# Kernel optimization log

Hardware: AMD Instinct MI355X
Metric: run time of the kernel (lower is better)

## Reference

```python
import jax, jax.numpy as jnp
import numpy as np

N_NODES = 50000


def gcn_conv(x, W, b, src, dst, n_nodes):
    # PyG GCNConv: y = D^-1/2 (A + I) D^-1/2 (x @ W) + b, with D counting self-loops
    h = x @ W                                             # [N, out]
    deg = jnp.ones((n_nodes,), h.dtype).at[dst].add(1.0)  # in-degree + self-loop
    dinv = jax.lax.rsqrt(deg)
    norm = dinv[src] * dinv[dst]                          # [E]
    msg = h[src] * norm[:, None]                          # [E, out]
    out = jnp.zeros_like(h).at[dst].add(msg)              # scatter-add over edges
    out = out + h * (dinv * dinv)[:, None]                # self-loop contribution
    return out + b


def setup_inputs() -> dict:
    key = jax.random.key(0)
    k = jax.random.split(key, 7)
    d_in, d_hid, d_out = 128, 128, 64
    x = jax.random.normal(k[0], (N_NODES, d_in), jnp.float32)
    edge_index = jax.random.randint(k[1], (2, 800000), 0, N_NODES, jnp.int64)
    s1 = 1.0 / np.sqrt(d_in)
    s2 = 1.0 / np.sqrt(d_hid)
    W1 = jax.random.uniform(k[2], (d_in, d_hid), jnp.float32, -s1, s1)
    b1 = jnp.zeros((d_hid,), jnp.float32)
    W2 = jax.random.uniform(k[3], (d_hid, d_out), jnp.float32, -s2, s2)
    b2 = jnp.zeros((d_out,), jnp.float32)
    return {"x": x, "edge_index": edge_index, "W1": W1, "b1": b1, "W2": W2, "b2": b2}


def reference(x, edge_index, W1, b1, W2, b2):
    src, dst = edge_index[0], edge_index[1]
    h = jax.nn.relu(gcn_conv(x, W1, b1, src, dst, N_NODES))
    h = gcn_conv(h, W2, b2, src, dst, N_NODES)
    return jax.nn.log_softmax(h, axis=1)
```

## Files before the change

kernel.cpp:

```cpp
#include <hip/hip_runtime.h>
#include <hip/hip_bf16.h>
#include <math.h>


typedef unsigned int uint32;
typedef unsigned short ushort16;
typedef __attribute__((ext_vector_type(8))) short bf16x8;
typedef __attribute__((ext_vector_type(4))) float f32x4;

__device__ inline unsigned short f2bf_rne(float f) {
    uint32 x = __float_as_uint(f);
    uint32 r = (x + 0x7fffu + ((x >> 16) & 1u)) >> 16;
    return (unsigned short)r;
}
__device__ inline uint32 pack_bf16x2(float a, float b) {
    return (uint32)f2bf_rne(a) | ((uint32)f2bf_rne(b) << 16);
}
__device__ inline float2 unpack_bf16x2(uint32 u) {
    float2 r;
    r.x = __uint_as_float(u << 16);
    r.y = __uint_as_float(u & 0xffff0000u);
    return r;
}

#define NHB 128

__global__ __launch_bounds__(256) void hist_conv_k(const int* __restrict__ dst, int E,
                                                   int NW, int chunk,
                                                   uint32* __restrict__ counts_pb,
                                                   ushort16* __restrict__ rankx,
                                                   const float* __restrict__ W1,
                                                   const float* __restrict__ W2,
                                                   unsigned short* __restrict__ W1t,
                                                   unsigned short* __restrict__ W2t) {
    const int tid = threadIdx.x;
    if ((int)blockIdx.x >= NHB) {
        int idx = ((int)blockIdx.x - NHB) * 256 + tid;
        if (idx < 128 * 128) {
            int ns = idx >> 7, k = idx & 127;
            int t = ns >> 4, m = ns & 15;
            int col = 32 * (t >> 1) + 2 * m + (t & 1);
            W1t[idx] = f2bf_rne(W1[k * 128 + col]);
        } else {
            int i2 = idx - 128 * 128;
            if (i2 < 64 * 128) {
                int ns = i2 >> 7, k = i2 & 127;
                int t = ns >> 4, m = ns & 15;
                int col = 32 * (t >> 1) + 2 * m + (t & 1);
                W2t[i2] = f2bf_rne(W2[k * 64 + col]);
            }
        }
        return;
    }
    extern __shared__ uint32 sh[];
    const int b = blockIdx.x;
    for (int i = tid; i < NW; i += 256) sh[i] = 0;
    __syncthreads();
    const int e0 = b * chunk;
    const int e1 = min(E, e0 + chunk);
    int e = e0 + tid;
    for (; e + 768 < e1; e += 1024) {
        int d0 = dst[e];
        int d1 = dst[e + 256];
        int d2 = dst[e + 512];
        int d3 = dst[e + 768];
        uint32 o0 = atomicAdd(&sh[d0 >> 1], (d0 & 1) ? 0x10000u : 1u);
        uint32 o1 = atomicAdd(&sh[d1 >> 1], (d1 & 1) ? 0x10000u : 1u);
        uint32 o2 = atomicAdd(&sh[d2 >> 1], (d2 & 1) ? 0x10000u : 1u);
        uint32 o3 = atomicAdd(&sh[d3 >> 1], (d3 & 1) ? 0x10000u : 1u);
        rankx[e]       = (ushort16)((d0 & 1) ? (o0 >> 16) : (o0 & 0xffffu));
        rankx[e + 256] = (ushort16)((d1 & 1) ? (o1 >> 16) : (o1 & 0xffffu));
        rankx[e + 512] = (ushort16)((d2 & 1) ? (o2 >> 16) : (o2 & 0xffffu));
        rankx[e + 768] = (ushort16)((d3 & 1) ? (o3 >> 16) : (o3 & 0xffffu));
    }
    for (; e < e1; e += 256) {
        int d = dst[e];
        uint32 o = atomicAdd(&sh[d >> 1], (d & 1) ? 0x10000u : 1u);
        rankx[e] = (ushort16)((d & 1) ? (o >> 16) : (o & 0xffffu));
    }
    __syncthreads();
    uint32* dstp = counts_pb + (size_t)b * NW;
    for (int i = tid; i < NW; i += 256) dstp[i] = sh[i];
}

__global__ __launch_bounds__(256) void scan2_k(const uint32* __restrict__ counts_pb,
                                               int N, int NW,
                                               ushort16* __restrict__ basecum,
                                               int* __restrict__ exscan,
                                               int* __restrict__ blocksum,
                                               float* __restrict__ dinv) {
    __shared__ int sd[256];
    const int tid = threadIdx.x;
    const int n   = blockIdx.x * 256 + tid;
    const int nc  = n < N ? n : N - 1;
    const int w   = nc >> 1;
    const bool hi = (nc & 1) != 0;
    int cum = 0;
    for (int bb = 0; bb < NHB; bb += 16) {
        uint32 wv[16];
#pragma unroll
        for (int j = 0; j < 16; ++j)
            wv[j] = counts_pb[(size_t)(bb + j) * NW + w];
#pragma unroll
        for (int j = 0; j < 16; ++j) {
            int c = hi ? (int)(wv[j] >> 16) : (int)(wv[j] & 0xffffu);
            if (n < N) basecum[(size_t)(bb + j) * N + n] = (ushort16)cum;
            cum += c;
        }
    }
    int v = (n < N) ? cum : 0;
    if (n < N) dinv[n] = rsqrtf((float)(v + 1));
    sd[tid] = v;
    __syncthreads();
    for (int off = 1; off < 256; off <<= 1) {
        int t = (tid >= off) ? sd[tid - off] : 0;
        __syncthreads();
        sd[tid] += t;
        __syncthreads();
    }
    if (n < N) exscan[n] = sd[tid] - v;
    if (tid == 255) blocksum[blockIdx.x] = sd[255];
}

__global__ __launch_bounds__(256) void fill_gemm1_k(const int* __restrict__ src,
                                                    const int* __restrict__ dst, int E,
                                                    int chunk, int N,
                                                    const ushort16* __restrict__ rankx,
                                                    const ushort16* __restrict__ basecum,
                                                    const int* __restrict__ blocksum,
                                                    int NB,
                                                    const int* __restrict__ exscan,
                                                    int* __restrict__ offsets,
                                                    ushort16* __restrict__ csr_src,
                                                    const float* __restrict__ X,
                                                    const unsigned short* __restrict__ Wt,
                                                    const float* __restrict__ dinv,
                                                    uint32* __restrict__ Yu, int Nrows) {
    __shared__ int sd[256];
    __shared__ int ebs[256];
    __shared__ int total;
    if ((int)blockIdx.x < 256) {
        const int f   = blockIdx.x;
        const int tid = threadIdx.x;
        int v = (tid < NB) ? blocksum[tid] : 0;
        sd[tid] = v;
        __syncthreads();
        for (int off = 1; off < 256; off <<= 1) {
            int t = (tid >= off) ? sd[tid - off] : 0;
            __syncthreads();
            sd[tid] += t;
            __syncthreads();
        }
        ebs[tid] = sd[tid] - v;
        if (tid == 255) total = sd[255];
        __syncthreads();
        int g = f * 256 + tid;
        if (g < N) offsets[g] = ebs[g >> 8] + exscan[g];
        else if (g == N) offsets[N] = total;
        const int b  = f >> 1;
        const ushort16* bc = basecum + (size_t)b * N;
        const int q2 = chunk >> 1;
        const int e0 = b * chunk + (f & 1) * q2;
        const int e1 = min(E, e0 + q2);
        int e = e0 + tid;
        for (; e + 768 < e1; e += 1024) {
#pragma unroll
            for (int j = 0; j < 4; ++j) {
                int ej = e + j * 256;
                int d = dst[ej];
                int pos = ebs[d >> 8] + exscan[d] + (int)bc[d] + (int)rankx[ej];
                csr_src[pos] = (ushort16)src[ej];
            }
        }
        for (; e < e1; e += 256) {
            int d = dst[e];
            int pos = ebs[d >> 8] + exscan[d] + (int)bc[d] + (int)rankx[e];
            csr_src[pos] = (ushort16)src[e];
        }
        return;
    }
    constexpr int NCOL = 128;
    constexpr int NT = NCOL / 16;
    const int tid  = threadIdx.x;
    const int wave = tid >> 6;
    const int lane = tid & 63;
    const int m16  = lane & 15;
    const int q    = lane >> 4;
    const int r0   = ((int)blockIdx.x - 256) * 64 + wave * 16;

    int arow = r0 + m16;
    if (arow >= Nrows) arow = Nrows - 1;

    bf16x8 afrag[4];
#pragma unroll
    for (int kb = 0; kb < 4; ++kb) {
        const float* p = &X[(size_t)arow * 128 + kb * 32 + q * 8];
        float4 u0 = *(const float4*)p;
        float4 u1 = *(const float4*)(p + 4);
        bf16x8 a;
        a[0] = (short)f2bf_rne(u0.x); a[1] = (short)f2bf_rne(u0.y);
        a[2] = (short)f2bf_rne(u0.z); a[3] = (short)f2bf_rne(u0.w);
        a[4] = (short)f2bf_rne(u1.x); a[5] = (short)f2bf_rne(u1.y);
        a[6] = (short)f2bf_rne(u1.z); a[7] = (short)f2bf_rne(u1.w);
        afrag[kb] = a;
    }

    f32x4 acc[NT];
#pragma unroll
    for (int t = 0; t < NT; ++t) acc[t] = (f32x4){0.f, 0.f, 0.f, 0.f};
#pragma unroll
    for (int t = 0; t < NT; ++t) {
        const unsigned short* Bp = &Wt[(size_t)(t * 16 + m16) * 128 + q * 8];
#pragma unroll
        for (int kb = 0; kb < 4; ++kb) {
            bf16x8 bfrag = *(const bf16x8*)&Bp[kb * 32];
            acc[t] = __builtin_amdgcn_mfma_f32_16x16x32_bf16(afrag[kb], bfrag, acc[t], 0, 0, 0);
        }
    }
#pragma unroll
    for (int i = 0; i < 4; ++i) {
        int row = r0 + q * 4 + i;
        if (row < Nrows) {
            float dn = dinv[row];
#pragma unroll
            for (int u = 0; u < NT / 2; ++u)
                Yu[(size_t)row * (NCOL / 2) + u * 16 + m16] =
                    pack_bf16x2(acc[2 * u][i] * dn, acc[2 * u + 1][i] * dn);
        }
    }
}

__global__ __launch_bounds__(256, 8) void agg1_gemm2_k(const unsigned short* __restrict__ hs,
                                                       const int* __restrict__ offsets,
                                                       const ushort16* __restrict__ csr_src,
                                                       const float* __restrict__ dinv,
                                                       const float* __restrict__ b1,
                                                       const unsigned short* __restrict__ W2t,
                                                       uint32* __restrict__ Yu, int N) {
    __shared__ uint32 srow[16 * 68];
    const int tid  = threadIdx.x;
    const int w    = tid >> 6;
    const int lane = tid & 63;
    const int base = (int)blockIdx.x * 16;
    const uint32* T = (const uint32*)hs;
    const float2 bb = ((const float2*)b1)[lane];
#pragma unroll
    for (int which = 0; which < 4; ++which) {
        const int node = base + 4 * w + which;
        uint32 packed = 0;
        if (node < N) {
            const int start = offsets[node];
            const int end   = offsets[node + 1];
            const float dn  = dinv[node];
            float2 self = unpack_bf16x2(T[(size_t)node * 64 + lane]);
            float ax0 = self.x, ay0 = self.y;
            float ax1 = 0.f, ay1 = 0.f, ax2 = 0.f, ay2 = 0.f, ax3 = 0.f, ay3 = 0.f;
            int p = start;
            for (; p + 7 < end; p += 8) {
                int s0 = csr_src[p];
                int s1 = csr_src[p + 1];
                int s2 = csr_src[p + 2];
                int s3 = csr_src[p + 3];
                int s4 = csr_src[p + 4];
                int s5 = csr_src[p + 5];
                int s6 = csr_src[p + 6];
                int s7 = csr_src[p + 7];
                uint32 u0 = T[(size_t)s0 * 64 + lane];
                uint32 u1 = T[(size_t)s1 * 64 + lane];
                uint32 u2 = T[(size_t)s2 * 64 + lane];
                uint32 u3 = T[(size_t)s3 * 64 + lane];
                uint32 u4 = T[(size_t)s4 * 64 + lane];
                uint32 u5 = T[(size_t)s5 * 64 + lane];
                uint32 u6 = T[(size_t)s6 * 64 + lane];
                uint32 u7 = T[(size_t)s7 * 64 + lane];
                float2 f0 = unpack_bf16x2(u0);
                float2 f1 = unpack_bf16x2(u1);
                float2 f2 = unpack_bf16x2(u2);
                float2 f3 = unpack_bf16x2(u3);
                float2 f4 = unpack_bf16x2(u4);
                float2 f5 = unpack_bf16x2(u5);
                float2 f6 = unpack_bf16x2(u6);
                float2 f7 = unpack_bf16x2(u7);
                ax0 += f0.x + f4.x; ay0 += f0.y + f4.y;
                ax1 += f1.x + f5.x; ay1 += f1.y + f5.y;
                ax2 += f2.x + f6.x; ay2 += f2.y + f6.y;
                ax3 += f3.x + f7.x; ay3 += f3.y + f7.y;
            }
            for (; p + 3 < end; p += 4) {
                int s0 = csr_src[p];
                int s1 = csr_src[p + 1];
                int s2 = csr_src[p + 2];
                int s3 = csr_src[p + 3];
                float2 f0 = unpack_bf16x2(T[(size_t)s0 * 64 + lane]);
                float2 f1 = unpack_bf16x2(T[(size_t)s1 * 64 + lane]);
                float2 f2 = unpack_bf16x2(T[(size_t)s2 * 64 + lane]);
                float2 f3 = unpack_bf16x2(T[(size_t)s3 * 64 + lane]);
                ax0 += f0.x; ay0 += f0.y;
                ax1 += f1.x; ay1 += f1.y;
                ax2 += f2.x; ay2 += f2.y;
                ax3 += f3.x; ay3 += f3.y;
            }
            for (; p < end; ++p) {
                float2 f = unpack_bf16x2(T[(size_t)csr_src[p] * 64 + lane]);
                ax1 += f.x; ay1 += f.y;
            }
            float vx = ((ax0 + ax1) + (ax2 + ax3)) * dn + bb.x;
            float vy = ((ay0 + ay1) + (ay2 + ay3)) * dn + bb.y;
            vx = vx > 0.f ? vx : 0.f;
            vy = vy > 0.f ? vy : 0.f;
            packed = pack_bf16x2(vx, vy);
        }
        srow[(4 * w + which) * 68 + lane] = packed;
    }
    __syncthreads();
    if (w < 2) {
        const int pp  = w;
        const int m16 = lane & 15;
        const int q   = lane >> 4;
        bf16x8 afrag[4];
#pragma unroll
        for (int kb = 0; kb < 4; ++kb)
            afrag[kb] = *(const bf16x8*)&srow[m16 * 68 + kb * 16 + q * 4];
        f32x4 acc0 = (f32x4){0.f, 0.f, 0.f, 0.f};
        f32x4 acc1 = (f32x4){0.f, 0.f, 0.f, 0.f};
        const unsigned short* Bp0 = &W2t[(size_t)((2 * pp) * 16 + m16) * 128 + q * 8];
        const unsigned short* Bp1 = &W2t[(size_t)((2 * pp + 1) * 16 + m16) * 128 + q * 8];
#pragma unroll
        for (int kb = 0; kb < 4; ++kb) {
            bf16x8 b0  = *(const bf16x8*)&Bp0[kb * 32];
            bf16x8 b1f = *(const bf16x8*)&Bp1[kb * 32];
            acc0 = __builtin_amdgcn_mfma_f32_16x16x32_bf16(afrag[kb], b0, acc0, 0, 0, 0);
            acc1 = __builtin_amdgcn_mfma_f32_16x16x32_bf16(afrag[kb], b1f, acc1, 0, 0, 0);
        }
#pragma unroll
        for (int i = 0; i < 4; ++i) {
            int row = base + q * 4 + i;
            if (row < N) {
                float dn2 = dinv[row];
                Yu[(size_t)row * 32 + pp * 16 + m16] =
                    pack_bf16x2(acc0[i] * dn2, acc1[i] * dn2);
            }
        }
    }
}

__global__ __launch_bounds__(256) void agg2_k(const unsigned short* __restrict__ hs,
                                              const int* __restrict__ offsets,
                                              const ushort16* __restrict__ csr_src,
                                              const float* __restrict__ dinv,
                                              const float* __restrict__ b2,
                                              float* __restrict__ out, int N) {
    const int tid  = threadIdx.x;
    const int node = blockIdx.x * 8 + (tid >> 5);
    const int l    = tid & 31;
    if (node >= N) return;
    const uint32* T = (const uint32*)hs;
    const int start = offsets[node];
    const int end   = offsets[node + 1];
    const float dn  = dinv[node];
    float2 self = unpack_bf16x2(T[(size_t)node * 32 + l]);
    float ax0 = self.x, ay0 = self.y;
    float ax1 = 0.f, ay1 = 0.f, ax2 = 0.f, ay2 = 0.f, ax3 = 0.f, ay3 = 0.f;
    int p = start;
    for (; p + 7 < end; p += 8) {
        int s0 = csr_src[p];
        int s1 = csr_src[p + 1];
        int s2 = csr_src[p + 2];
        int s3 = csr_src[p + 3];
        int s4 = csr_src[p + 4];
        int s5 = csr_src[p + 5];
        int s6 = csr_src[p + 6];
        int s7 = csr_src[p + 7];
        uint32 u0 = T[(size_t)s0 * 32 + l];
        uint32 u1 = T[(size_t)s1 * 32 + l];
        uint32 u2 = T[(size_t)s2 * 32 + l];
        uint32 u3 = T[(size_t)s3 * 32 + l];
        uint32 u4 = T[(size_t)s4 * 32 + l];
        uint32 u5 = T[(size_t)s5 * 32 + l];
        uint32 u6 = T[(size_t)s6 * 32 + l];
        uint32 u7 = T[(size_t)s7 * 32 + l];
        float2 f0 = unpack_bf16x2(u0);
        float2 f1 = unpack_bf16x2(u1);
        float2 f2 = unpack_bf16x2(u2);
        float2 f3 = unpack_bf16x2(u3);
        float2 f4 = unpack_bf16x2(u4);
        float2 f5 = unpack_bf16x2(u5);
        float2 f6 = unpack_bf16x2(u6);
        float2 f7 = unpack_bf16x2(u7);
        ax0 += f0.x + f4.x; ay0 += f0.y + f4.y;
        ax1 += f1.x + f5.x; ay1 += f1.y + f5.y;
        ax2 += f2.x + f6.x; ay2 += f2.y + f6.y;
        ax3 += f3.x + f7.x; ay3 += f3.y + f7.y;
    }
    for (; p + 3 < end; p += 4) {
        int s0 = csr_src[p];
        int s1 = csr_src[p + 1];
        int s2 = csr_src[p + 2];
        int s3 = csr_src[p + 3];
        float2 f0 = unpack_bf16x2(T[(size_t)s0 * 32 + l]);
        float2 f1 = unpack_bf16x2(T[(size_t)s1 * 32 + l]);
        float2 f2 = unpack_bf16x2(T[(size_t)s2 * 32 + l]);
        float2 f3 = unpack_bf16x2(T[(size_t)s3 * 32 + l]);
        ax0 += f0.x; ay0 += f0.y;
        ax1 += f1.x; ay1 += f1.y;
        ax2 += f2.x; ay2 += f2.y;
        ax3 += f3.x; ay3 += f3.y;
    }
    for (; p < end; ++p) {
        float2 f = unpack_bf16x2(T[(size_t)csr_src[p] * 32 + l]);
        ax1 += f.x; ay1 += f.y;
    }
    float2 bb = ((const float2*)b2)[l];
    float vx = ((ax0 + ax1) + (ax2 + ax3)) * dn + bb.x;
    float vy = ((ay0 + ay1) + (ay2 + ay3)) * dn + bb.y;
    float m = fmaxf(vx, vy);
#pragma unroll
    for (int off = 16; off > 0; off >>= 1) m = fmaxf(m, __shfl_xor(m, off, 64));
    float ex = __expf(vx - m) + __expf(vy - m);
    float ssum = ex;
#pragma unroll
    for (int off = 16; off > 0; off >>= 1) ssum += __shfl_xor(ssum, off, 64);
    float lse = m + __logf(ssum);
    float2 o = {vx - lse, vy - lse};
    ((float2*)out)[(size_t)node * 32 + l] = o;
}

extern "C" void kernel_launch(void* const* d_in, const int* in_sizes, int n_in,
                              void* d_out, int out_size, void* d_ws, size_t ws_size,
                              hipStream_t stream) {
    const float* x  = (const float*)d_in[0];
    const int*   ei = (const int*)d_in[1];
    const float* W1 = (const float*)d_in[2];
    const float* b1 = (const float*)d_in[3];
    const float* W2 = (const float*)d_in[4];
    const float* b2 = (const float*)d_in[5];
    float* out = (float*)d_out;

    const int N = in_sizes[0] / 128;
    const int E = in_sizes[1] / 2;
    const int* src = ei;
    const int* dst = ei + E;
    const int NB = (N + 255) / 256;
    const int NW = (N + 1) / 2;
    const int chunk = (E + NHB - 1) / NHB;

    char* ws = (char*)d_ws;
    auto alloc = [&](size_t bytes) -> char* {
        char* p = ws;
        ws += (bytes + 255) & ~(size_t)255;
        return p;
    };
    unsigned short* h1  = (unsigned short*)alloc((size_t)N * 128 * 2);
    unsigned short* h2  = (unsigned short*)alloc((size_t)N * 64 * 2);
    uint32* counts_pb = (uint32*)alloc((size_t)NHB * NW * 4);
    ushort16* basecum = (ushort16*)alloc((size_t)NHB * N * 2);
    ushort16* rankx   = (ushort16*)alloc((size_t)E * 2);
    ushort16* csr_src = (ushort16*)alloc((size_t)E * 2);
    float* dinv     = (float*)alloc((size_t)N * 4);
    int*   exscan   = (int*)alloc((size_t)N * 4);
    int*   blocksum = (int*)alloc((size_t)NB * 4);
    int*   offsets  = (int*)alloc((size_t)(N + 1) * 4);
    unsigned short* W1t = (unsigned short*)alloc(128 * 128 * 2);
    unsigned short* W2t = (unsigned short*)alloc(64 * 128 * 2);

    const int GB = (N + 63) / 64;
    const int CB = (128 * 128 + 64 * 128 + 255) / 256;

    hist_conv_k<<<NHB + CB, 256, NW * 4, stream>>>(dst, E, NW, chunk, counts_pb, rankx,
                                                   W1, W2, W1t, W2t);
    scan2_k<<<NB, 256, 0, stream>>>(counts_pb, N, NW, basecum, exscan, blocksum, dinv);
    fill_gemm1_k<<<256 + GB, 256, 0, stream>>>(src, dst, E, chunk, N, rankx, basecum,
                                               blocksum, NB, exscan, offsets, csr_src,
                                               x, W1t, dinv, (uint32*)h1, N);
    agg1_gemm2_k<<<(N + 15) / 16, 256, 0, stream>>>(h1, offsets, csr_src, dinv, b1,
                                                    W2t, (uint32*)h2, N);
    agg2_k<<<(N + 7) / 8, 256, 0, stream>>>(h2, offsets, csr_src, dinv, b2, out, N);
}
```

Before: 191.6 us.

## Pad CSR rows to multiples of 8 with a zero dummy node and quarter histogram shared memory

```diff
diff --git a/kernel.cpp b/kernel.cpp
--- a/kernel.cpp
+++ b/kernel.cpp
@@ -34,8 +34,8 @@
                                                    unsigned short* __restrict__ W1t,
                                                    unsigned short* __restrict__ W2t) {
     const int tid = threadIdx.x;
-    if ((int)blockIdx.x >= NHB) {
-        int idx = ((int)blockIdx.x - NHB) * 256 + tid;
+    if ((int)blockIdx.x >= 4 * NHB) {
+        int idx = ((int)blockIdx.x - 4 * NHB) * 256 + tid;
         if (idx < 128 * 128) {
             int ns = idx >> 7, k = idx & 127;
             int t = ns >> 4, m = ns & 15;
@@ -53,10 +53,15 @@
         return;
     }
     extern __shared__ uint32 sh[];
-    const int b = blockIdx.x;
-    for (int i = tid; i < NW; i += 256) sh[i] = 0;
+    const int hb  = blockIdx.x >> 2;
+    const int qt  = blockIdx.x & 3;
+    const int NWq = (NW + 3) >> 2;
+    const int qlo = qt * NWq;
+    const int qhi = min(NW, qlo + NWq);
+    const int qn  = qhi - qlo;
+    for (int i = tid; i < qn; i += 256) sh[i] = 0;
     __syncthreads();
-    const int e0 = b * chunk;
+    const int e0 = hb * chunk;
     const int e1 = min(E, e0 + chunk);
     int e = e0 + tid;
     for (; e + 768 < e1; e += 1024) {
@@ -64,23 +69,35 @@
         int d1 = dst[e + 256];
         int d2 = dst[e + 512];
         int d3 = dst[e + 768];
-        uint32 o0 = atomicAdd(&sh[d0 >> 1], (d0 & 1) ? 0x10000u : 1u);
-        uint32 o1 = atomicAdd(&sh[d1 >> 1], (d1 & 1) ? 0x10000u : 1u);
-        uint32 o2 = atomicAdd(&sh[d2 >> 1], (d2 & 1) ? 0x10000u : 1u);
-        uint32 o3 = atomicAdd(&sh[d3 >> 1], (d3 & 1) ? 0x10000u : 1u);
-        rankx[e]       = (ushort16)((d0 & 1) ? (o0 >> 16) : (o0 & 0xffffu));
-        rankx[e + 256] = (ushort16)((d1 & 1) ? (o1 >> 16) : (o1 & 0xffffu));
-        rankx[e + 512] = (ushort16)((d2 & 1) ? (o2 >> 16) : (o2 & 0xffffu));
-        rankx[e + 768] = (ushort16)((d3 & 1) ? (o3 >> 16) : (o3 & 0xffffu));
+        int w0 = d0 >> 1, w1 = d1 >> 1, w2 = d2 >> 1, w3 = d3 >> 1;
+        if (w0 >= qlo && w0 < qhi) {
+            uint32 o = atomicAdd(&sh[w0 - qlo], (d0 & 1) ? 0x10000u : 1u);
+            rankx[e] = (ushort16)((d0 & 1) ? (o >> 16) : (o & 0xffffu));
+        }
+        if (w1 >= qlo && w1 < qhi) {
+            uint32 o = atomicAdd(&sh[w1 - qlo], (d1 & 1) ? 0x10000u : 1u);
+            rankx[e + 256] = (ushort16)((d1 & 1) ? (o >> 16) : (o & 0xffffu));
+        }
+        if (w2 >= qlo && w2 < qhi) {
+            uint32 o = atomicAdd(&sh[w2 - qlo], (d2 & 1) ? 0x10000u : 1u);
+            rankx[e + 512] = (ushort16)((d2 & 1) ? (o >> 16) : (o & 0xffffu));
+        }
+        if (w3 >= qlo && w3 < qhi) {
+            uint32 o = atomicAdd(&sh[w3 - qlo], (d3 & 1) ? 0x10000u : 1u);
+            rankx[e + 768] = (ushort16)((d3 & 1) ? (o >> 16) : (o & 0xffffu));
+        }
     }
     for (; e < e1; e += 256) {
         int d = dst[e];
-        uint32 o = atomicAdd(&sh[d >> 1], (d & 1) ? 0x10000u : 1u);
-        rankx[e] = (ushort16)((d & 1) ? (o >> 16) : (o & 0xffffu));
+        int w = d >> 1;
+        if (w >= qlo && w < qhi) {
+            uint32 o = atomicAdd(&sh[w - qlo], (d & 1) ? 0x10000u : 1u);
+            rankx[e] = (ushort16)((d & 1) ? (o >> 16) : (o & 0xffffu));
+        }
     }
     __syncthreads();
-    uint32* dstp = counts_pb + (size_t)b * NW;
-    for (int i = tid; i < NW; i += 256) dstp[i] = sh[i];
+    uint32* dstp = counts_pb + (size_t)hb * NW + qlo;
+    for (int i = tid; i < qn; i += 256) dstp[i] = sh[i];
 }
 
 __global__ __launch_bounds__(256) void scan2_k(const uint32* __restrict__ counts_pb,
@@ -88,7 +105,8 @@
                                                ushort16* __restrict__ basecum,
                                                int* __restrict__ exscan,
                                                int* __restrict__ blocksum,
-                                               float* __restrict__ dinv) {
+                                               float* __restrict__ dinv,
+                                               ushort16* __restrict__ degs) {
     __shared__ int sd[256];
     const int tid = threadIdx.x;
     const int n   = blockIdx.x * 256 + tid;
@@ -109,8 +127,12 @@
         }
     }
     int v = (n < N) ? cum : 0;
-    if (n < N) dinv[n] = rsqrtf((float)(v + 1));
-    sd[tid] = v;
+    if (n < N) {
+        dinv[n] = rsqrtf((float)(v + 1));
+        degs[n] = (ushort16)v;
+    }
+    int vp = (v + 7) & ~7;
+    sd[tid] = vp;
     __syncthreads();
     for (int off = 1; off < 256; off <<= 1) {
         int t = (tid >= off) ? sd[tid - off] : 0;
@@ -118,7 +140,7 @@
         sd[tid] += t;
         __syncthreads();
     }
-    if (n < N) exscan[n] = sd[tid] - v;
+    if (n < N) exscan[n] = sd[tid] - vp;
     if (tid == 255) blocksum[blockIdx.x] = sd[255];
 }
 
@@ -130,6 +152,7 @@
                                                     const int* __restrict__ blocksum,
                                                     int NB,
                                                     const int* __restrict__ exscan,
+                                                    const ushort16* __restrict__ degs,
                                                     int* __restrict__ offsets,
                                                     ushort16* __restrict__ csr_src,
                                                     const float* __restrict__ X,
@@ -155,8 +178,15 @@
         if (tid == 255) total = sd[255];
         __syncthreads();
         int g = f * 256 + tid;
-        if (g < N) offsets[g] = ebs[g >> 8] + exscan[g];
-        else if (g == N) offsets[N] = total;
+        if (g < N) {
+            int off = ebs[g >> 8] + exscan[g];
+            offsets[g] = off;
+            int dg = degs[g];
+            int pl = (dg + 7) & ~7;
+            for (int k = dg; k < pl; ++k) csr_src[off + k] = (ushort16)N;
+        } else if (g == N) {
+            offsets[N] = total;
+        }
         const int b  = f >> 1;
         const ushort16* bc = basecum + (size_t)b * N;
         const int q2 = chunk >> 1;
@@ -187,6 +217,8 @@
     const int m16  = lane & 15;
     const int q    = lane >> 4;
     const int r0   = ((int)blockIdx.x - 256) * 64 + wave * 16;
+
+    if ((int)blockIdx.x == 256 && tid < 64) Yu[(size_t)Nrows * (NCOL / 2) + tid] = 0;
 
     int arow = r0 + m16;
     if (arow >= Nrows) arow = Nrows - 1;
@@ -244,6 +276,7 @@
     const int base = (int)blockIdx.x * 16;
     const uint32* T = (const uint32*)hs;
     const float2 bb = ((const float2*)b1)[lane];
+    if (blockIdx.x == 0 && w == 2 && lane < 32) Yu[(size_t)N * 32 + lane] = 0;
 #pragma unroll
     for (int which = 0; which < 4; ++which) {
         const int node = base + 4 * w + which;
@@ -256,15 +289,17 @@
             float ax0 = self.x, ay0 = self.y;
             float ax1 = 0.f, ay1 = 0.f, ax2 = 0.f, ay2 = 0.f, ax3 = 0.f, ay3 = 0.f;
             int p = start;
-            for (; p + 7 < end; p += 8) {
-                int s0 = csr_src[p];
-                int s1 = csr_src[p + 1];
-                int s2 = csr_src[p + 2];
-                int s3 = csr_src[p + 3];
-                int s4 = csr_src[p + 4];
-                int s5 = csr_src[p + 5];
-                int s6 = csr_src[p + 6];
-                int s7 = csr_src[p + 7];
+            for (; p + 15 < end; p += 16) {
+                uint4 ia = *(const uint4*)&csr_src[p];
+                uint4 ib = *(const uint4*)&csr_src[p + 8];
+                int s0 = ia.x & 0xffff, s1 = ia.x >> 16;
+                int s2 = ia.y & 0xffff, s3 = ia.y >> 16;
+                int s4 = ia.z & 0xffff, s5 = ia.z >> 16;
+                int s6 = ia.w & 0xffff, s7 = ia.w >> 16;
+                int s8 = ib.x & 0xffff, s9 = ib.x >> 16;
+                int sa = ib.y & 0xffff, sb = ib.y >> 16;
+                int sc = ib.z & 0xffff, sd = ib.z >> 16;
+                int se = ib.w & 0xffff, sf = ib.w >> 16;
                 uint32 u0 = T[(size_t)s0 * 64 + lane];
                 uint32 u1 = T[(size_t)s1 * 64 + lane];
                 uint32 u2 = T[(size_t)s2 * 64 + lane];
@@ -273,36 +308,53 @@
                 uint32 u5 = T[(size_t)s5 * 64 + lane];
                 uint32 u6 = T[(size_t)s6 * 64 + lane];
                 uint32 u7 = T[(size_t)s7 * 64 + lane];
-                float2 f0 = unpack_bf16x2(u0);
-                float2 f1 = unpack_bf16x2(u1);
-                float2 f2 = unpack_bf16x2(u2);
-                float2 f3 = unpack_bf16x2(u3);
-                float2 f4 = unpack_bf16x2(u4);
-                float2 f5 = unpack_bf16x2(u5);
-                float2 f6 = unpack_bf16x2(u6);
-                float2 f7 = unpack_bf16x2(u7);
+                uint32 u8 = T[(size_t)s8 * 64 + lane];
+                uint32 u9 = T[(size_t)s9 * 64 + lane];
+                uint32 ua = T[(size_t)sa * 64 + lane];
+                uint32 ub = T[(size_t)sb * 64 + lane];
+                uint32 uc = T[(size_t)sc * 64 + lane];
+                uint32 ud = T[(size_t)sd * 64 + lane];
+                uint32 ue = T[(size_t)se * 64 + lane];
+                uint32 uf = T[(size_t)sf * 64 + lane];
+                float2 f0 = unpack_bf16x2(u0), f1 = unpack_bf16x2(u1);
+                float2 f2 = unpack_bf16x2(u2), f3 = unpack_bf16x2(u3);
+                float2 f4 = unpack_bf16x2(u4), f5 = unpack_bf16x2(u5);
+                float2 f6 = unpack_bf16x2(u6), f7 = unpack_bf16x2(u7);
+                float2 f8 = unpack_bf16x2(u8), f9 = unpack_bf16x2(u9);
+                float2 fa = unpack_bf16x2(ua), fb = unpack_bf16x2(ub);
+                float2 fc = unpack_bf16x2(uc), fd = unpack_bf16x2(ud);
+                float2 fe = unpack_bf16x2(ue), ff = unpack_bf16x2(uf);
+                ax0 += (f0.x + f4.x) + (f8.x + fc.x);
+                ay0 += (f0.y + f4.y) + (f8.y + fc.y);
+                ax1 += (f1.x + f5.x) + (f9.x + fd.x);
+                ay1 += (f1.y + f5.y) + (f9.y + fd.y);
+                ax2 += (f2.x + f6.x) + (fa.x + fe.x);
+                ay2 += (f2.y + f6.y) + (fa.y + fe.y);
+                ax3 += (f3.x + f7.x) + (fb.x + ff.x);
+                ay3 += (f3.y + f7.y) + (fb.y + ff.y);
+            }
+            for (; p + 7 < end; p += 8) {
+                uint4 ia = *(const uint4*)&csr_src[p];
+                int s0 = ia.x & 0xffff, s1 = ia.x >> 16;
+                int s2 = ia.y & 0xffff, s3 = ia.y >> 16;
+                int s4 = ia.z & 0xffff, s5 = ia.z >> 16;
+                int s6 = ia.w & 0xffff, s7 = ia.w >> 16;
+                uint32 u0 = T[(size_t)s0 * 64 + lane];
+                uint32 u1 = T[(size_t)s1 * 64 + lane];
+                uint32 u2 = T[(size_t)s2 * 64 + lane];
+                uint32 u3 = T[(size_t)s3 * 64 + lane];
+                uint32 u4 = T[(size_t)s4 * 64 + lane];
+                uint32 u5 = T[(size_t)s5 * 64 + lane];
+                uint32 u6 = T[(size_t)s6 * 64 + lane];
+                uint32 u7 = T[(size_t)s7 * 64 + lane];
+                float2 f0 = unpack_bf16x2(u0), f1 = unpack_bf16x2(u1);
+                float2 f2 = unpack_bf16x2(u2), f3 = unpack_bf16x2(u3);
+                float2 f4 = unpack_bf16x2(u4), f5 = unpack_bf16x2(u5);
+                float2 f6 = unpack_bf16x2(u6), f7 = unpack_bf16x2(u7);
                 ax0 += f0.x + f4.x; ay0 += f0.y + f4.y;
                 ax1 += f1.x + f5.x; ay1 += f1.y + f5.y;
                 ax2 += f2.x + f6.x; ay2 += f2.y + f6.y;
                 ax3 += f3.x + f7.x; ay3 += f3.y + f7.y;
-            }
-            for (; p + 3 < end; p += 4) {
-                int s0 = csr_src[p];
-                int s1 = csr_src[p + 1];
-                int s2 = csr_src[p + 2];
-                int s3 = csr_src[p + 3];
-                float2 f0 = unpack_bf16x2(T[(size_t)s0 * 64 + lane]);
-                float2 f1 = unpack_bf16x2(T[(size_t)s1 * 64 + lane]);
-                float2 f2 = unpack_bf16x2(T[(size_t)s2 * 64 + lane]);
-                float2 f3 = unpack_bf16x2(T[(size_t)s3 * 64 + lane]);
-                ax0 += f0.x; ay0 += f0.y;
-                ax1 += f1.x; ay1 += f1.y;
-                ax2 += f2.x; ay2 += f2.y;
-                ax3 += f3.x; ay3 += f3.y;
-            }
-            for (; p < end; ++p) {
-                float2 f = unpack_bf16x2(T[(size_t)csr_src[p] * 64 + lane]);
-                ax1 += f.x; ay1 += f.y;
             }
             float vx = ((ax0 + ax1) + (ax2 + ax3)) * dn + bb.x;
             float vy = ((ay0 + ay1) + (ay2 + ay3)) * dn + bb.y;
@@ -344,12 +396,12 @@
     }
 }
 
-__global__ __launch_bounds__(256) void agg2_k(const unsigned short* __restrict__ hs,
-                                              const int* __restrict__ offsets,
-                                              const ushort16* __restrict__ csr_src,
-                                              const float* __restrict__ dinv,
-                                              const float* __restrict__ b2,
-                                              float* __restrict__ out, int N) {
+__global__ __launch_bounds__(256, 8) void agg2_k(const unsigned short* __restrict__ hs,
+                                                 const int* __restrict__ offsets,
+                                                 const ushort16* __restrict__ csr_src,
+                                                 const float* __restrict__ dinv,
+                                                 const float* __restrict__ b2,
+                                                 float* __restrict__ out, int N) {
     const int tid  = threadIdx.x;
     const int node = blockIdx.x * 8 + (tid >> 5);
     const int l    = tid & 31;
@@ -362,15 +414,17 @@
     float ax0 = self.x, ay0 = self.y;
     float ax1 = 0.f, ay1 = 0.f, ax2 = 0.f, ay2 = 0.f, ax3 = 0.f, ay3 = 0.f;
     int p = start;
-    for (; p + 7 < end; p += 8) {
-        int s0 = csr_src[p];
-        int s1 = csr_src[p + 1];
-        int s2 = csr_src[p + 2];
-        int s3 = csr_src[p + 3];
-        int s4 = csr_src[p + 4];
-        int s5 = csr_src[p + 5];
-        int s6 = csr_src[p + 6];
-        int s7 = csr_src[p + 7];
+    for (; p + 15 < end; p += 16) {
+        uint4 ia = *(const uint4*)&csr_src[p];
+        uint4 ib = *(const uint4*)&csr_src[p + 8];
+        int s0 = ia.x & 0xffff, s1 = ia.x >> 16;
+        int s2 = ia.y & 0xffff, s3 = ia.y >> 16;
+        int s4 = ia.z & 0xffff, s5 = ia.z >> 16;
+        int s6 = ia.w & 0xffff, s7 = ia.w >> 16;
+        int s8 = ib.x & 0xffff, s9 = ib.x >> 16;
+        int sa = ib.y & 0xffff, sb = ib.y >> 16;
+        int sc = ib.z & 0xffff, sd = ib.z >> 16;
+        int se = ib.w & 0xffff, sf = ib.w >> 16;
         uint32 u0 = T[(size_t)s0 * 32 + l];
         uint32 u1 = T[(size_t)s1 * 32 + l];
         uint32 u2 = T[(size_t)s2 * 32 + l];
@@ -379,36 +433,53 @@
         uint32 u5 = T[(size_t)s5 * 32 + l];
         uint32 u6 = T[(size_t)s6 * 32 + l];
         uint32 u7 = T[(size_t)s7 * 32 + l];
-        float2 f0 = unpack_bf16x2(u0);
-        float2 f1 = unpack_bf16x2(u1);
-        float2 f2 = unpack_bf16x2(u2);
-        float2 f3 = unpack_bf16x2(u3);
-        float2 f4 = unpack_bf16x2(u4);
-        float2 f5 = unpack_bf16x2(u5);
-        float2 f6 = unpack_bf16x2(u6);
-        float2 f7 = unpack_bf16x2(u7);
+        uint32 u8 = T[(size_t)s8 * 32 + l];
+        uint32 u9 = T[(size_t)s9 * 32 + l];
+        uint32 ua = T[(size_t)sa * 32 + l];
+        uint32 ub = T[(size_t)sb * 32 + l];
+        uint32 uc = T[(size_t)sc * 32 + l];
+        uint32 ud = T[(size_t)sd * 32 + l];
+        uint32 ue = T[(size_t)se * 32 + l];
+        uint32 uf = T[(size_t)sf * 32 + l];
+        float2 f0 = unpack_bf16x2(u0), f1 = unpack_bf16x2(u1);
+        float2 f2 = unpack_bf16x2(u2), f3 = unpack_bf16x2(u3);
+        float2 f4 = unpack_bf16x2(u4), f5 = unpack_bf16x2(u5);
+        float2 f6 = unpack_bf16x2(u6), f7 = unpack_bf16x2(u7);
+        float2 f8 = unpack_bf16x2(u8), f9 = unpack_bf16x2(u9);
+        float2 fa = unpack_bf16x2(ua), fb = unpack_bf16x2(ub);
+        float2 fc = unpack_bf16x2(uc), fd = unpack_bf16x2(ud);
+        float2 fe = unpack_bf16x2(ue), ff = unpack_bf16x2(uf);
+        ax0 += (f0.x + f4.x) + (f8.x + fc.x);
+        ay0 += (f0.y + f4.y) + (f8.y + fc.y);
+        ax1 += (f1.x + f5.x) + (f9.x + fd.x);
+        ay1 += (f1.y + f5.y) + (f9.y + fd.y);
+        ax2 += (f2.x + f6.x) + (fa.x + fe.x);
+        ay2 += (f2.y + f6.y) + (fa.y + fe.y);
+        ax3 += (f3.x + f7.x) + (fb.x + ff.x);
+        ay3 += (f3.y + f7.y) + (fb.y + ff.y);
+    }
+    for (; p + 7 < end; p += 8) {
+        uint4 ia = *(const uint4*)&csr_src[p];
+        int s0 = ia.x & 0xffff, s1 = ia.x >> 16;
+        int s2 = ia.y & 0xffff, s3 = ia.y >> 16;
+        int s4 = ia.z & 0xffff, s5 = ia.z >> 16;
+        int s6 = ia.w & 0xffff, s7 = ia.w >> 16;
+        uint32 u0 = T[(size_t)s0 * 32 + l];
+        uint32 u1 = T[(size_t)s1 * 32 + l];
+        uint32 u2 = T[(size_t)s2 * 32 + l];
+        uint32 u3 = T[(size_t)s3 * 32 + l];
+        uint32 u4 = T[(size_t)s4 * 32 + l];
+        uint32 u5 = T[(size_t)s5 * 32 + l];
+        uint32 u6 = T[(size_t)s6 * 32 + l];
+        uint32 u7 = T[(size_t)s7 * 32 + l];
+        float2 f0 = unpack_bf16x2(u0), f1 = unpack_bf16x2(u1);
+        float2 f2 = unpack_bf16x2(u2), f3 = unpack_bf16x2(u3);
+        float2 f4 = unpack_bf16x2(u4), f5 = unpack_bf16x2(u5);
+        float2 f6 = unpack_bf16x2(u6), f7 = unpack_bf16x2(u7);
         ax0 += f0.x + f4.x; ay0 += f0.y + f4.y;
         ax1 += f1.x + f5.x; ay1 += f1.y + f5.y;
         ax2 += f2.x + f6.x; ay2 += f2.y + f6.y;
         ax3 += f3.x + f7.x; ay3 += f3.y + f7.y;
-    }
-    for (; p + 3 < end; p += 4) {
-        int s0 = csr_src[p];
-        int s1 = csr_src[p + 1];
-        int s2 = csr_src[p + 2];
-        int s3 = csr_src[p + 3];
-        float2 f0 = unpack_bf16x2(T[(size_t)s0 * 32 + l]);
-        float2 f1 = unpack_bf16x2(T[(size_t)s1 * 32 + l]);
-        float2 f2 = unpack_bf16x2(T[(size_t)s2 * 32 + l]);
-        float2 f3 = unpack_bf16x2(T[(size_t)s3 * 32 + l]);
-        ax0 += f0.x; ay0 += f0.y;
-        ax1 += f1.x; ay1 += f1.y;
-        ax2 += f2.x; ay2 += f2.y;
-        ax3 += f3.x; ay3 += f3.y;
-    }
-    for (; p < end; ++p) {
-        float2 f = unpack_bf16x2(T[(size_t)csr_src[p] * 32 + l]);
-        ax1 += f.x; ay1 += f.y;
     }
     float2 bb = ((const float2*)b2)[l];
     float vx = ((ax0 + ax1) + (ax2 + ax3)) * dn + bb.x;
@@ -442,6 +513,7 @@
     const int* dst = ei + E;
     const int NB = (N + 255) / 256;
     const int NW = (N + 1) / 2;
+    const int NWq = (NW + 3) >> 2;
     const int chunk = (E + NHB - 1) / NHB;
 
     char* ws = (char*)d_ws;
@@ -450,28 +522,30 @@
         ws += (bytes + 255) & ~(size_t)255;
         return p;
     };
-    unsigned short* h1  = (unsigned short*)alloc((size_t)N * 128 * 2);
-    unsigned short* h2  = (unsigned short*)alloc((size_t)N * 64 * 2);
+    unsigned short* h1  = (unsigned short*)alloc((size_t)(N + 1) * 128 * 2);
+    unsigned short* h2  = (unsigned short*)alloc((size_t)(N + 1) * 64 * 2);
     uint32* counts_pb = (uint32*)alloc((size_t)NHB * NW * 4);
     ushort16* basecum = (ushort16*)alloc((size_t)NHB * N * 2);
     ushort16* rankx   = (ushort16*)alloc((size_t)E * 2);
-    ushort16* csr_src = (ushort16*)alloc((size_t)E * 2);
+    ushort16* csr_src = (ushort16*)alloc(((size_t)E + 8 * (size_t)N) * 2);
     float* dinv     = (float*)alloc((size_t)N * 4);
     int*   exscan   = (int*)alloc((size_t)N * 4);
     int*   blocksum = (int*)alloc((size_t)NB * 4);
     int*   offsets  = (int*)alloc((size_t)(N + 1) * 4);
+    ushort16* degs  = (ushort16*)alloc((size_t)N * 2);
     unsigned short* W1t = (unsigned short*)alloc(128 * 128 * 2);
     unsigned short* W2t = (unsigned short*)alloc(64 * 128 * 2);
 
     const int GB = (N + 63) / 64;
     const int CB = (128 * 128 + 64 * 128 + 255) / 256;
 
-    hist_conv_k<<<NHB + CB, 256, NW * 4, stream>>>(dst, E, NW, chunk, counts_pb, rankx,
-                                                   W1, W2, W1t, W2t);
-    scan2_k<<<NB, 256, 0, stream>>>(counts_pb, N, NW, basecum, exscan, blocksum, dinv);
+    hist_conv_k<<<4 * NHB + CB, 256, NWq * 4, stream>>>(dst, E, NW, chunk, counts_pb,
+                                                        rankx, W1, W2, W1t, W2t);
+    scan2_k<<<NB, 256, 0, stream>>>(counts_pb, N, NW, basecum, exscan, blocksum, dinv,
+                                    degs);
     fill_gemm1_k<<<256 + GB, 256, 0, stream>>>(src, dst, E, chunk, N, rankx, basecum,
-                                               blocksum, NB, exscan, offsets, csr_src,
-                                               x, W1t, dinv, (uint32*)h1, N);
+                                               blocksum, NB, exscan, degs, offsets,
+                                               csr_src, x, W1t, dinv, (uint32*)h1, N);
     agg1_gemm2_k<<<(N + 15) / 16, 256, 0, stream>>>(h1, offsets, csr_src, dinv, b1,
                                                     W2t, (uint32*)h2, N);
     agg2_k<<<(N + 7) / 8, 256, 0, stream>>>(h2, offsets, csr_src, dinv, b2, out, N);
```

Result: faster. 180.0 us (-6.1%).
